# Kernel tuning notes

Hardware: AMD Instinct MI355X
Metric: run time of the kernel (lower is better)

The kernel has to match this reference:

```python
import jax, jax.numpy as jnp
import numpy as np

# ----- module constants (from init_kwargs) -----
N = 1024          # Np = [N, N]
NZ = 16           # number of slices (O.shape[3])
NA = 0.65         # objective NA
WL = 0.5          # wavelength (um)
PS = 6.5          # camera pixel size (um)
MAG = 20.0        # magnification
PS_EFF = PS / MAG
DZ = 10.0 * PS / MAG                 # slice spacing (code overwrites wl/na**2)
KAPPA = 2.0 * np.pi * DZ / WL        # imag part of self.k
K = np.complex64(1j * KAPPA)         # self.k as a complex scalar


def _grids():
    c = (np.arange(N) - N // 2) * PS_EFF
    xx, yy = np.meshgrid(c, c)                       # spatial grids
    f = (np.arange(N) - N // 2) / (PS_EFF * N)
    uxx, uyy = np.meshgrid(f, f)                     # frequency grids
    return xx, yy, uxx, uyy

_XX, _YY, _UXX, _UYY = _grids()
_URR = _UXX ** 2 + _UYY ** 2
_PC = (_URR < (NA / WL) ** 2).astype(np.float64)     # centered pupil


def _fresnel(dz):
    # genFrensel: band-limited angular-spectrum kernel, stored in fft order
    kz = np.sqrt(np.maximum(_PC * ((1.0 / WL) ** 2 - _URR), 0.0))
    kern = _PC * np.exp(1j * 2.0 * np.pi * dz * kz)
    return jnp.asarray(np.fft.fftshift(kern).astype(np.complex64))

PUPIL = jnp.asarray(np.fft.fftshift(_PC).astype(np.complex64))   # fft order
PROPKERN = _fresnel(DZ)
PROPKERN_FOCUS = _fresnel(-DZ * (NZ - 1) / 2.0)
XX = jnp.asarray(_XX, jnp.float32)
YY = jnp.asarray(_YY, jnp.float32)


def _prop(u, kern):
    # torch.fft / torch.ifft pair == unnormalized fft2 / normalized ifft2
    return jnp.fft.ifft2(jnp.fft.fft2(u) * kern)


def _plane_wave(na_illum):
    dfx = 1.0 / (PS_EFF * N)
    tilt = jnp.round((na_illum / WL) / dfx) * dfx    # snap tilt to freq grid
    phase = 2.0 * np.pi * (tilt[0] * XX + tilt[1] * YY)
    return jnp.exp(1j * phase)                        # complex64


def _ms_grad(O, intensity, na_illum):
    """Faithful translation of Multislice.grad. O: [N,N,NZ] complex64."""
    T = jnp.exp(K * O)                                # per-slice transmittance
    u = _plane_wave(na_illum)
    # forward multislice propagation
    for zz in range(NZ):
        u = T[..., zz] * u
        if zz < NZ - 1:
            u = _prop(u, PROPKERN)
    # refocus to stack center, apply pupil
    u_ref = _prop(u, PROPKERN_FOCUS)
    u_pup = _prop(u_ref, PUPIL)
    # amplitude-replacement residual
    abs_field = jnp.abs(u_pup)
    comp = jnp.sqrt(intensity) * u_pup / abs_field
    residual = u_pup - comp
    # back-propagate residual
    u_bp = _prop(residual, jnp.conj(PUPIL))
    u_bp = _prop(u_bp, jnp.conj(PROPKERN_FOCUS))
    # reverse slice loop accumulating per-slice gradient
    grads = [None] * NZ
    for zz in range(NZ - 1, -1, -1):
        grads[zz] = u_bp * jnp.conj(u) * jnp.conj(T[..., zz]) * np.conj(K)
        if zz > 0:
            u_bp = _prop(u_bp * jnp.conj(T[..., zz]), jnp.conj(PROPKERN))
            u = _prop(u, jnp.conj(PROPKERN))
            u = u / T[..., zz - 1]
    return jnp.stack(grads, axis=-1)                  # [N,N,NZ] complex


def setup_inputs() -> dict:
    key = jax.random.key(0)
    k1, k2, k3 = jax.random.split(key, 3)
    # small-valued object so exp(i*KAPPA*O) stays bounded (KAPPA ~ 40.8)
    x = jax.random.normal(k1, (N, N, 2, NZ), jnp.float32) * 0.01
    meas = jax.random.uniform(k2, (N, N), jnp.float32) + 0.1
    na_illum = jax.random.uniform(k3, (2,), jnp.float32) * 0.2
    alpha = jnp.full((1,), 0.01, jnp.float32)
    return {"x": x, "meas": meas, "na_illum": na_illum, "alpha": alpha}


def reference(x, meas, na_illum, alpha):
    # forward: x + step(x) = x - alpha * grad(x, meas, na_illum)
    O = x[..., 0, :] + 1j * x[..., 1, :]              # [N,N,NZ] complex64
    g = _ms_grad(O, meas, na_illum)
    out = O - alpha[0] * g
    return jnp.stack((out.real, out.imag), axis=2)    # back to [N,N,2,NZ]
```

## Files before the change

kernel.cpp:

```cpp
#include <hip/hip_runtime.h>
#include <math.h>


#define NN (1024*1024)
#define KAPPA 40.840704496667314f
#define TWO_PI_F 6.2831853071795865f
#define DFX_D 0.0030048076923076925
#define RRCUT 187177
#define F(i) ((i) + ((i)>>4))

#define JT 0
#define JT_WP 1
#define JN 2
#define JRESID 3

__device__ __forceinline__ float2 cmulf(float2 a, float2 b){
    return make_float2(a.x*b.x - a.y*b.y, a.x*b.y + a.y*b.x);
}
__device__ __forceinline__ float2 cmulcj(float2 a, float2 b){
    return make_float2(a.x*b.x + a.y*b.y, a.y*b.x - a.x*b.y);
}
__device__ __forceinline__ float2 f2add(float2 a, float2 b){ return make_float2(a.x+b.x, a.y+b.y); }
__device__ __forceinline__ float2 f2sub(float2 a, float2 b){ return make_float2(a.x-b.x, a.y-b.y); }

__device__ __forceinline__ void fill_tw(float2* tw, int tid){
    #pragma unroll
    for (int k = tid; k < 512; k += 256){
        float s, c; sincosf(-(float)k * (TWO_PI_F/1024.0f), &s, &c);
        tw[k] = make_float2(c, s);
    }
}

__device__ __forceinline__ void dif_ph1(float2 r[8], const float2* tw, int lane){
    float2 a, d;
    #pragma unroll
    for (int k=0;k<4;++k){
        a=r[k]; d=f2sub(r[k],r[k+4]);
        r[k]=f2add(a,r[k+4]);
        r[k+4]=cmulf(d, tw[lane+128*k]);
    }
    float2 w20 = tw[lane<<1], w21 = tw[(lane+128)<<1];
    a=r[0]; d=f2sub(r[0],r[2]); r[0]=f2add(a,r[2]); r[2]=cmulf(d,w20);
    a=r[1]; d=f2sub(r[1],r[3]); r[1]=f2add(a,r[3]); r[3]=cmulf(d,w21);
    a=r[4]; d=f2sub(r[4],r[6]); r[4]=f2add(a,r[6]); r[6]=cmulf(d,w20);
    a=r[5]; d=f2sub(r[5],r[7]); r[5]=f2add(a,r[7]); r[7]=cmulf(d,w21);
    float2 w3 = tw[lane<<2];
    a=r[0]; d=f2sub(r[0],r[1]); r[0]=f2add(a,r[1]); r[1]=cmulf(d,w3);
    a=r[2]; d=f2sub(r[2],r[3]); r[2]=f2add(a,r[3]); r[3]=cmulf(d,w3);
    a=r[4]; d=f2sub(r[4],r[5]); r[4]=f2add(a,r[5]); r[5]=cmulf(d,w3);
    a=r[6]; d=f2sub(r[6],r[7]); r[6]=f2add(a,r[7]); r[7]=cmulf(d,w3);
}
__device__ __forceinline__ void dit_ph1(float2 r[8], const float2* tw, int lane){
    float2 a, b;
    float2 w3 = tw[lane<<2];
    a=r[0]; b=cmulcj(r[1],w3); r[0]=f2add(a,b); r[1]=f2sub(a,b);
    a=r[2]; b=cmulcj(r[3],w3); r[2]=f2add(a,b); r[3]=f2sub(a,b);
    a=r[4]; b=cmulcj(r[5],w3); r[4]=f2add(a,b); r[5]=f2sub(a,b);
    a=r[6]; b=cmulcj(r[7],w3); r[6]=f2add(a,b); r[7]=f2sub(a,b);
    float2 w20 = tw[lane<<1], w21 = tw[(lane+128)<<1];
    a=r[0]; b=cmulcj(r[2],w20); r[0]=f2add(a,b); r[2]=f2sub(a,b);
    a=r[1]; b=cmulcj(r[3],w21); r[1]=f2add(a,b); r[3]=f2sub(a,b);
    a=r[4]; b=cmulcj(r[6],w20); r[4]=f2add(a,b); r[6]=f2sub(a,b);
    a=r[5]; b=cmulcj(r[7],w21); r[5]=f2add(a,b); r[7]=f2sub(a,b);
    #pragma unroll
    for (int k=0;k<4;++k){
        a=r[k]; b=cmulcj(r[k+4], tw[lane+128*k]);
        r[k]=f2add(a,b); r[k+4]=f2sub(a,b);
    }
}
__device__ __forceinline__ void dif_ph2(float2 r[8], const float2* tw, int m0){
    float2 a, d;
    #pragma unroll
    for (int k=0;k<4;++k){
        a=r[k]; d=f2sub(r[k],r[k+4]);
        r[k]=f2add(a,r[k+4]);
        r[k+4]=cmulf(d, tw[(m0+16*k)<<3]);
    }
    float2 w40 = tw[m0<<4], w41 = tw[(m0+16)<<4];
    a=r[0]; d=f2sub(r[0],r[2]); r[0]=f2add(a,r[2]); r[2]=cmulf(d,w40);
    a=r[1]; d=f2sub(r[1],r[3]); r[1]=f2add(a,r[3]); r[3]=cmulf(d,w41);
    a=r[4]; d=f2sub(r[4],r[6]); r[4]=f2add(a,r[6]); r[6]=cmulf(d,w40);
    a=r[5]; d=f2sub(r[5],r[7]); r[5]=f2add(a,r[7]); r[7]=cmulf(d,w41);
    float2 w5 = tw[m0<<5];
    a=r[0]; d=f2sub(r[0],r[1]); r[0]=f2add(a,r[1]); r[1]=cmulf(d,w5);
    a=r[2]; d=f2sub(r[2],r[3]); r[2]=f2add(a,r[3]); r[3]=cmulf(d,w5);
    a=r[4]; d=f2sub(r[4],r[5]); r[4]=f2add(a,r[5]); r[5]=cmulf(d,w5);
    a=r[6]; d=f2sub(r[6],r[7]); r[6]=f2add(a,r[7]); r[7]=cmulf(d,w5);
}
__device__ __forceinline__ void dit_ph2(float2 r[8], const float2* tw, int m0){
    float2 a, b;
    float2 w5 = tw[m0<<5];
    a=r[0]; b=cmulcj(r[1],w5); r[0]=f2add(a,b); r[1]=f2sub(a,b);
    a=r[2]; b=cmulcj(r[3],w5); r[2]=f2add(a,b); r[3]=f2sub(a,b);
    a=r[4]; b=cmulcj(r[5],w5); r[4]=f2add(a,b); r[5]=f2sub(a,b);
    a=r[6]; b=cmulcj(r[7],w5); r[6]=f2add(a,b); r[7]=f2sub(a,b);
    float2 w40 = tw[m0<<4], w41 = tw[(m0+16)<<4];
    a=r[0]; b=cmulcj(r[2],w40); r[0]=f2add(a,b); r[2]=f2sub(a,b);
    a=r[1]; b=cmulcj(r[3],w41); r[1]=f2add(a,b); r[3]=f2sub(a,b);
    a=r[4]; b=cmulcj(r[6],w40); r[4]=f2add(a,b); r[6]=f2sub(a,b);
    a=r[5]; b=cmulcj(r[7],w41); r[5]=f2add(a,b); r[7]=f2sub(a,b);
    #pragma unroll
    for (int k=0;k<4;++k){
        a=r[k]; b=cmulcj(r[k+4], tw[(m0+16*k)<<3]);
        r[k]=f2add(a,b); r[k+4]=f2sub(a,b);
    }
}
__device__ __forceinline__ void dif_reg(float2 r[8]){
    const float C = 0.70710678118654752f;
    float2 a,d;
    a=r[0]; d=f2sub(r[0],r[4]); r[0]=f2add(a,r[4]); r[4]=d;
    a=r[1]; d=f2sub(r[1],r[5]); r[1]=f2add(a,r[5]); r[5]=make_float2(C*(d.x+d.y), C*(d.y-d.x));
    a=r[2]; d=f2sub(r[2],r[6]); r[2]=f2add(a,r[6]); r[6]=make_float2(d.y, -d.x);
    a=r[3]; d=f2sub(r[3],r[7]); r[3]=f2add(a,r[7]); r[7]=make_float2(C*(d.y-d.x), -C*(d.x+d.y));
    a=r[0]; r[0]=f2add(a,r[2]); r[2]=f2sub(a,r[2]);
    a=r[1]; d=f2sub(r[1],r[3]); r[1]=f2add(a,r[3]); r[3]=make_float2(d.y,-d.x);
    a=r[4]; r[4]=f2add(a,r[6]); r[6]=f2sub(a,r[6]);
    a=r[5]; d=f2sub(r[5],r[7]); r[5]=f2add(a,r[7]); r[7]=make_float2(d.y,-d.x);
    a=r[0]; r[0]=f2add(a,r[1]); r[1]=f2sub(a,r[1]);
    a=r[2]; r[2]=f2add(a,r[3]); r[3]=f2sub(a,r[3]);
    a=r[4]; r[4]=f2add(a,r[5]); r[5]=f2sub(a,r[5]);
    a=r[6]; r[6]=f2add(a,r[7]); r[7]=f2sub(a,r[7]);
}
__device__ __forceinline__ void dit_reg(float2 r[8]){
    const float C = 0.70710678118654752f;
    float2 a,b,t;
    a=r[0]; r[0]=f2add(a,r[1]); r[1]=f2sub(a,r[1]);
    a=r[2]; r[2]=f2add(a,r[3]); r[3]=f2sub(a,r[3]);
    a=r[4]; r[4]=f2add(a,r[5]); r[5]=f2sub(a,r[5]);
    a=r[6]; r[6]=f2add(a,r[7]); r[7]=f2sub(a,r[7]);
    a=r[0]; r[0]=f2add(a,r[2]); r[2]=f2sub(a,r[2]);
    a=r[1]; t=r[3]; b=make_float2(-t.y, t.x); r[1]=f2add(a,b); r[3]=f2sub(a,b);
    a=r[4]; r[4]=f2add(a,r[6]); r[6]=f2sub(a,r[6]);
    a=r[5]; t=r[7]; b=make_float2(-t.y, t.x); r[5]=f2add(a,b); r[7]=f2sub(a,b);
    a=r[0]; r[0]=f2add(a,r[4]); r[4]=f2sub(a,r[4]);
    a=r[1]; t=r[5]; b=make_float2(C*(t.x-t.y), C*(t.x+t.y)); r[1]=f2add(a,b); r[5]=f2sub(a,b);
    a=r[2]; t=r[6]; b=make_float2(-t.y, t.x); r[2]=f2add(a,b); r[6]=f2sub(a,b);
    a=r[3]; t=r[7]; b=make_float2(-C*(t.x+t.y), C*(t.x-t.y)); r[3]=f2add(a,b); r[7]=f2sub(a,b);
}

__device__ __forceinline__ void st128l(float2* L, int ro, int lane, const float2 r[8]){
    #pragma unroll
    for (int k=0;k<8;++k) L[F(ro + lane + 128*k)] = r[k];
}
__device__ __forceinline__ void ld128l(const float2* L, int ro, int lane, float2 r[8]){
    #pragma unroll
    for (int k=0;k<8;++k) r[k] = L[F(ro + lane + 128*k)];
}
__device__ __forceinline__ void st16l(float2* L, int ro, int lane, const float2 r[8]){
    int b = lane>>4, m0 = lane&15, q = ro + 128*b + m0;
    #pragma unroll
    for (int k=0;k<8;++k) L[F(q + 16*k)] = r[k];
}
__device__ __forceinline__ void ld16l(const float2* L, int ro, int lane, float2 r[8]){
    int b = lane>>4, m0 = lane&15, q = ro + 128*b + m0;
    #pragma unroll
    for (int k=0;k<8;++k) r[k] = L[F(q + 16*k)];
}
__device__ __forceinline__ void st8l(float2* L, int ro, int lane, const float2 r[8]){
    int q = ro + 8*lane;
    #pragma unroll
    for (int i=0;i<8;++i) L[F(q + i)] = r[i];
}
__device__ __forceinline__ void ldfold_dif(const float2* L, int ro, int lane,
                                           const float2* tw, float2 r[8]){
    int rr = lane>>1, sub = lane&1, q = ro + 16*rr;
    #pragma unroll
    for (int i=0;i<8;++i){
        float2 x = L[F(q + i)];
        float2 y = L[F(q + 8 + i)];
        r[i] = sub ? cmulf(f2sub(x,y), tw[i<<6]) : f2add(x,y);
    }
}
__device__ __forceinline__ void ldfold_dit(const float2* L, int ro, int lane,
                                           const float2* tw, float2 r[8]){
    int b = lane>>4, m0 = lane&15, m0s = m0&7;
    float2 w = tw[m0s<<6];
    int q = ro + 128*b + m0s;
    #pragma unroll
    for (int k=0;k<8;++k){
        float2 x = L[F(q + 16*k)];
        float2 y = L[F(q + 16*k + 8)];
        float2 bb = cmulcj(y, w);
        r[k] = (m0 < 8) ? f2add(x,bb) : f2sub(x,bb);
    }
}
__device__ __forceinline__ void load8g(const float2* src, int lane, float2 r[8]){
    const float4* s4 = (const float4*)src + lane*4;
    #pragma unroll
    for (int m=0;m<4;++m){
        float4 v = s4[m];
        r[2*m]   = make_float2(v.x, v.y);
        r[2*m+1] = make_float2(v.z, v.w);
    }
}
__device__ __forceinline__ void twrite2(const float2* L, int tid, float2* dst,
                                        int r0, float s){
    #pragma unroll
    for (int k=0;k<4;++k){
        int c = tid + (k<<8);
        float2 a0 = L[F(c)], a1 = L[F(1024+c)];
        ((float4*)(dst + ((size_t)c<<10) + r0))[0] =
            make_float4(a0.x*s, a0.y*s, a1.x*s, a1.y*s);
    }
}

__global__ void __launch_bounds__(256) k_kern(float2* __restrict__ kp,
                                              float2* __restrict__ kf){
    int idx = blockIdx.x*256 + threadIdx.x;
    int j = idx >> 10, i = idx & 1023;
    int a = __brev((unsigned)i) >> 22;
    int b = __brev((unsigned)j) >> 22;
    int ra = a - (a >= 512 ? 1024 : 0);
    int rb = b - (b >= 512 ? 1024 : 0);
    int rr = ra*ra + rb*rb;
    float2 p = make_float2(0.f,0.f), f = make_float2(0.f,0.f);
    if (rr <= RRCUT){
        double urr = (double)rr * (DFX_D*DFX_D);
        double kz = sqrt(4.0 - urr);
        double s1,c1,s2,c2;
        sincos(6.283185307179586 * 3.25    * kz, &s1, &c1);
        sincos(6.283185307179586 * -24.375 * kz, &s2, &c2);
        p = make_float2((float)c1,(float)s1);
        f = make_float2((float)c2,(float)s2);
    }
    kp[idx] = p; kf[idx] = f;
}

__global__ void __launch_bounds__(256) k_T(const float4* __restrict__ x,
                                           float2* __restrict__ T){
    int idx = blockIdx.x*256 + threadIdx.x;
    const float4* xp = x + (size_t)idx*8;
    float4 v[8];
    #pragma unroll
    for (int k=0;k<8;++k) v[k] = xp[k];
    const float* fr = (const float*)v;
    #pragma unroll
    for (int z=0; z<16; ++z){
        float amp = __expf(-KAPPA*fr[16+z]);
        float s, c; __sincosf(KAPPA*fr[z], &s, &c);
        T[(size_t)z*NN + idx] = make_float2(amp*c, amp*s);
    }
}

__global__ void __launch_bounds__(256) k_head(float2* __restrict__ dst,
                                              const float2* __restrict__ T0,
                                              const float* __restrict__ nail){
    __shared__ float2 A[2176], B[2176], tw[512];
    const int tid = threadIdx.x;
    fill_tw(tw, tid);
    const int row = tid>>7, lane = tid&127, ro = row<<10, m0 = lane&15;
    const int r0 = blockIdx.x*2;
    const size_t gbase = ((size_t)(r0+row))<<10;
    float dfx = (float)DFX_D;
    float t0 = rintf(nail[0]*2.0f/dfx)*dfx;
    float t1 = rintf(nail[1]*2.0f/dfx)*dfx;
    float yv = (float)((r0+row) - 512) * 0.325f;
    float2 r[8];
    #pragma unroll
    for (int k=0;k<8;++k){
        int col = lane + 128*k;
        float2 tv = T0[gbase + col];
        float xv = (float)(col - 512) * 0.325f;
        float s0, c0; sincosf(TWO_PI_F*(t0*xv + t1*yv), &s0, &c0);
        r[k] = cmulf(make_float2(c0,s0), tv);
    }
    __syncthreads();
    dif_ph1(r, tw, lane);
    st128l(A, ro, lane, r); __syncthreads();
    ld16l(A, ro, lane, r); dif_ph2(r, tw, m0);
    st16l(B, ro, lane, r); __syncthreads();
    ldfold_dif(B, ro, lane, tw, r); dif_reg(r);
    st8l(A, ro, lane, r); __syncthreads();
    twrite2(A, tid, dst, r0, 1.0f);
}

__global__ void __launch_bounds__(256) k_pass2(
    const float2* __restrict__ srcA, float2* __restrict__ dstA,
    const float2* __restrict__ srcB, float2* __restrict__ dstB,
    const float2* __restrict__ km, int conj, int pupil)
{
    __shared__ float2 A[2176], B[2176], tw[512];
    const int tid = threadIdx.x;
    fill_tw(tw, tid);
    const int row = tid>>7, lane = tid&127, ro = row<<10, m0 = lane&15;
    int bid = blockIdx.x;
    const float2* src = srcA; float2* dst = dstA;
    if (srcB != nullptr && bid >= 512){ src = srcB; dst = dstB; bid -= 512; }
    const int r0 = bid*2;
    const int jrow = r0 + row;
    const float2* srcR = src + (((size_t)r0)<<10) + ro;
    float2 r[8];
    #pragma unroll
    for (int k=0;k<8;++k) r[k] = srcR[lane + 128*k];
    __syncthreads();
    dif_ph1(r, tw, lane);
    st128l(A, ro, lane, r); __syncthreads();
    ld16l(A, ro, lane, r); dif_ph2(r, tw, m0);
    st16l(B, ro, lane, r); __syncthreads();
    ldfold_dif(B, ro, lane, tw, r); dif_reg(r);
    if (pupil){
        int bb = __brev((unsigned)jrow) >> 22;
        int rb = bb - (bb >= 512 ? 1024 : 0);
        int rb2 = rb*rb;
        #pragma unroll
        for (int i=0;i<8;++i){
            int aa = __brev((unsigned)(8*lane+i)) >> 22;
            int ra = aa - (aa >= 512 ? 1024 : 0);
            if (ra*ra + rb2 > RRCUT) r[i] = make_float2(0.f,0.f);
        }
    } else {
        const float4* k4 = (const float4*)(km + (((size_t)jrow)<<10)) + lane*4;
        float sg = conj ? -1.0f : 1.0f;
        #pragma unroll
        for (int m=0;m<4;++m){
            float4 kv = k4[m];
            r[2*m]   = cmulf(r[2*m],   make_float2(kv.x, sg*kv.y));
            r[2*m+1] = cmulf(r[2*m+1], make_float2(kv.z, sg*kv.w));
        }
    }
    dit_reg(r);
    st8l(A, ro, lane, r); __syncthreads();
    ldfold_dit(A, ro, lane, tw, r); dit_ph2(r, tw, m0);
    st16l(B, ro, lane, r); __syncthreads();
    ld128l(B, ro, lane, r); dit_ph1(r, tw, lane);
    st128l(A, ro, lane, r); __syncthreads();
    twrite2(A, tid, dst, r0, 1.0f/1024.0f);
}

__global__ void __launch_bounds__(256) k_junc(
    const float2* __restrict__ src, float2* __restrict__ dst,
    const float2* __restrict__ Tz, float2* __restrict__ wp,
    const float* __restrict__ meas, int mode)
{
    __shared__ float2 A[2176], B[2176], tw[512];
    const int tid = threadIdx.x;
    fill_tw(tw, tid);
    const int row = tid>>7, lane = tid&127, ro = row<<10, m0 = lane&15;
    const int r0 = blockIdx.x*2;
    const size_t gbase = ((size_t)(r0+row))<<10;
    const float S = 1.0f/1024.0f;
    float2 r[8];
    load8g(src + (((size_t)r0)<<10) + ro, lane, r);
    dit_reg(r);
    st8l(A, ro, lane, r); __syncthreads();
    ldfold_dit(A, ro, lane, tw, r); dit_ph2(r, tw, m0);
    st16l(B, ro, lane, r); __syncthreads();
    ld128l(B, ro, lane, r); dit_ph1(r, tw, lane);
    #pragma unroll
    for (int k=0;k<8;++k){
        size_t g = gbase + lane + 128*k;
        float2 v = make_float2(S*r[k].x, S*r[k].y);
        if (mode == JT || mode == JT_WP){
            v = cmulf(v, Tz[g]);
            if (mode == JT_WP) wp[g] = v;
        } else if (mode == JRESID){
            float m = meas[g];
            float aamp = fmaxf(sqrtf(v.x*v.x + v.y*v.y), 1e-30f);
            float f = 1.0f - sqrtf(m)/aamp;
            v.x *= f; v.y *= f;
        }
        r[k] = v;
    }
    dif_ph1(r, tw, lane);
    st128l(A, ro, lane, r); __syncthreads();
    ld16l(A, ro, lane, r); dif_ph2(r, tw, m0);
    st16l(B, ro, lane, r); __syncthreads();
    ldfold_dif(B, ro, lane, tw, r); dif_reg(r);
    st8l(A, ro, lane, r); __syncthreads();
    twrite2(A, tid, dst, r0, 1.0f);
}

__global__ void __launch_bounds__(256) k_rev(
    const float2* __restrict__ srcU, float2* __restrict__ dstU,
    const float2* __restrict__ srcB, float2* __restrict__ dstB,
    float2* __restrict__ Tz, int headU)
{
    __shared__ float2 A[2176], B[2176], tw[512];
    const int tid = threadIdx.x;
    fill_tw(tw, tid);
    const int row = tid>>7, lane = tid&127, ro = row<<10, m0 = lane&15;
    const int r0 = blockIdx.x*2;
    const size_t gbase = ((size_t)(r0+row))<<10;
    const float S = 1.0f/1024.0f;
    float2 u[8], Tg[8], r[8];
    if (!headU){
        load8g(srcU + (((size_t)r0)<<10) + ro, lane, u);
        dit_reg(u);
        st8l(A, ro, lane, u); __syncthreads();
        ldfold_dit(A, ro, lane, tw, u); dit_ph2(u, tw, m0);
        st16l(B, ro, lane, u); __syncthreads();
        ld128l(B, ro, lane, u); dit_ph1(u, tw, lane);
        #pragma unroll
        for (int k=0;k<8;++k){ u[k].x *= S; u[k].y *= S; }
    } else {
        const float2* srcR = srcU + (((size_t)r0)<<10) + ro;
        #pragma unroll
        for (int k=0;k<8;++k) u[k] = srcR[lane + 128*k];
        __syncthreads();
    }
    #pragma unroll
    for (int k=0;k<8;++k) Tg[k] = Tz[gbase + lane + 128*k];
    #pragma unroll
    for (int k=0;k<8;++k){
        if (headU) r[k] = u[k];
        else {
            float inv = 1.0f/(Tg[k].x*Tg[k].x + Tg[k].y*Tg[k].y);
            float2 wc = cmulcj(u[k], Tg[k]);
            r[k] = make_float2(wc.x*inv, wc.y*inv);
        }
    }
    dif_ph1(r, tw, lane);
    st128l(A, ro, lane, r); __syncthreads();
    ld16l(A, ro, lane, r); dif_ph2(r, tw, m0);
    st16l(B, ro, lane, r); __syncthreads();
    ldfold_dif(B, ro, lane, tw, r); dif_reg(r);
    st8l(A, ro, lane, r); __syncthreads();
    twrite2(A, tid, dstU, r0, 1.0f);
    load8g(srcB + (((size_t)r0)<<10) + ro, lane, r);
    dit_reg(r);
    st8l(B, ro, lane, r); __syncthreads();
    ldfold_dit(B, ro, lane, tw, r); dit_ph2(r, tw, m0);
    st16l(A, ro, lane, r); __syncthreads();
    ld128l(A, ro, lane, r); dit_ph1(r, tw, lane);
    #pragma unroll
    for (int k=0;k<8;++k){
        float2 b = make_float2(S*r[k].x, S*r[k].y);
        float2 q = headU ? cmulcj(cmulcj(b, u[k]), Tg[k]) : cmulcj(b, u[k]);
        Tz[gbase + lane + 128*k] = make_float2(KAPPA*q.y, -KAPPA*q.x);
        r[k] = cmulcj(b, Tg[k]);
    }
    dif_ph1(r, tw, lane);
    st128l(B, ro, lane, r); __syncthreads();
    ld16l(B, ro, lane, r); dif_ph2(r, tw, m0);
    st16l(A, ro, lane, r); __syncthreads();
    ldfold_dif(A, ro, lane, tw, r); dif_reg(r);
    st8l(B, ro, lane, r); __syncthreads();
    twrite2(B, tid, dstB, r0, 1.0f);
}

__global__ void __launch_bounds__(256) k_tail(
    const float2* __restrict__ srcU, const float2* __restrict__ srcB,
    float2* __restrict__ G0)
{
    __shared__ float2 A[2176], B[2176], tw[512];
    const int tid = threadIdx.x;
    fill_tw(tw, tid);
    const int row = tid>>7, lane = tid&127, ro = row<<10, m0 = lane&15;
    const int r0 = blockIdx.x*2;
    const size_t gbase = ((size_t)(r0+row))<<10;
    const float S = 1.0f/1024.0f;
    float2 u[8], r[8];
    load8g(srcU + (((size_t)r0)<<10) + ro, lane, u);
    dit_reg(u);
    st8l(A, ro, lane, u); __syncthreads();
    ldfold_dit(A, ro, lane, tw, u); dit_ph2(u, tw, m0);
    st16l(B, ro, lane, u); __syncthreads();
    ld128l(B, ro, lane, u); dit_ph1(u, tw, lane);
    load8g(srcB + (((size_t)r0)<<10) + ro, lane, r);
    dit_reg(r);
    st8l(A, ro, lane, r); __syncthreads();
    ldfold_dit(A, ro, lane, tw, r); dit_ph2(r, tw, m0);
    st16l(B, ro, lane, r); __syncthreads();
    ld128l(B, ro, lane, r); dit_ph1(r, tw, lane);
    #pragma unroll
    for (int k=0;k<8;++k){
        float2 b = make_float2(S*r[k].x, S*r[k].y);
        float2 w = make_float2(S*u[k].x, S*u[k].y);
        float2 q = cmulcj(b, w);
        G0[gbase + lane + 128*k] = make_float2(KAPPA*q.y, -KAPPA*q.x);
    }
}

__global__ void __launch_bounds__(256) k_merge(const float4* __restrict__ x,
                                               const float2* __restrict__ G,
                                               const float* __restrict__ alpha,
                                               float4* __restrict__ out){
    int idx = blockIdx.x*256 + threadIdx.x;
    float al = alpha[0];
    const float4* xp = x + (size_t)idx*8;
    float4 xv[8];
    #pragma unroll
    for (int k=0;k<8;++k) xv[k] = xp[k];
    const float* fx = (const float*)xv;
    float o[32];
    #pragma unroll
    for (int z=0;z<16;++z){
        float2 g = G[(size_t)z*NN + idx];
        o[z]    = fx[z]    - al*g.x;
        o[16+z] = fx[16+z] - al*g.y;
    }
    float4* op = out + (size_t)idx*8;
    #pragma unroll
    for (int k=0;k<8;++k)
        op[k] = make_float4(o[4*k], o[4*k+1], o[4*k+2], o[4*k+3]);
}

extern "C" void kernel_launch(void* const* d_in, const int* in_sizes, int n_in,
                              void* d_out, int out_size, void* d_ws, size_t ws_size,
                              hipStream_t stream)
{
    const float* x     = (const float*)d_in[0];
    const float* meas  = (const float*)d_in[1];
    const float* nail  = (const float*)d_in[2];
    const float* alpha = (const float*)d_in[3];

    if (ws_size < (size_t)23*NN*sizeof(float2)) return;

    float2* W   = (float2*)d_ws;
    float2* T   = W;
    float2* KP  = W + (size_t)16*NN;
    float2* KF  = W + (size_t)17*NN;
    float2* U0  = W + (size_t)18*NN;
    float2* TAB = W + (size_t)19*NN;
    float2* TBB = W + (size_t)20*NN;
    float2* TAU = W + (size_t)21*NN;
    float2* TBU = W + (size_t)22*NN;

    k_kern<<<4096, 256, 0, stream>>>(KP, KF);
    k_T   <<<4096, 256, 0, stream>>>((const float4*)x, T);

    auto P2f = [&](const float2* km, int cj, int pup){
        k_pass2<<<512, 256, 0, stream>>>(TAB, TBB, nullptr, nullptr, km, cj, pup);
    };

    k_head<<<512, 256, 0, stream>>>(TAB, T, nail);
    P2f(KP, 0, 0);
    for (int z = 1; z <= 14; ++z){
        k_junc<<<512, 256, 0, stream>>>(TBB, TAB, T + (size_t)z*NN, nullptr, nullptr, JT);
        P2f(KP, 0, 0);
    }
    k_junc<<<512, 256, 0, stream>>>(TBB, TAB, T + (size_t)15*NN, U0, nullptr, JT_WP);
    P2f(KF, 0, 0);
    k_junc<<<512, 256, 0, stream>>>(TBB, TAB, nullptr, nullptr, nullptr, JN);
    P2f(nullptr, 0, 1);
    k_junc<<<512, 256, 0, stream>>>(TBB, TAB, nullptr, nullptr, meas, JRESID);
    P2f(nullptr, 1, 1);
    k_junc<<<512, 256, 0, stream>>>(TBB, TAB, nullptr, nullptr, nullptr, JN);
    P2f(KF, 1, 0);

    for (int zz = 15; zz >= 1; --zz){
        k_rev<<<512, 256, 0, stream>>>(zz == 15 ? U0 : TBU, TAU, TBB, TAB,
                                       T + (size_t)zz*NN, zz == 15 ? 1 : 0);
        k_pass2<<<1024, 256, 0, stream>>>(TAB, TBB, TAU, TBU, KP, 1, 0);
    }
    k_tail<<<512, 256, 0, stream>>>(TBU, TBB, T);

    k_merge<<<4096, 256, 0, stream>>>((const float4*)x, T, alpha, (float4*)d_out);
}
```

Measured before the change: 1.514 ms.

## Hoist global loads ahead of LDS FFT stages and widen elementwise kernels

Global loads of kernel coefficients, transmittance, measurements and the second FFT operand are issued before the shared-memory FFT phases in pass2, junc, rev and tail. Their latency can then overlap with compute and barriers instead of stalling afterwards. The T and merge kernels are rewritten so each thread handles a quarter or eighth of a pixel's slices, giving more threads and better-coalesced loads. The cost is higher register pressure from the extra live arrays, which may reduce occupancy.

```diff
diff --git a/kernel.cpp b/kernel.cpp
--- a/kernel.cpp
+++ b/kernel.cpp
@@ -229,16 +229,18 @@
 __global__ void __launch_bounds__(256) k_T(const float4* __restrict__ x,
                                            float2* __restrict__ T){
     int idx = blockIdx.x*256 + threadIdx.x;
-    const float4* xp = x + (size_t)idx*8;
-    float4 v[8];
-    #pragma unroll
-    for (int k=0;k<8;++k) v[k] = xp[k];
-    const float* fr = (const float*)v;
-    #pragma unroll
-    for (int z=0; z<16; ++z){
-        float amp = __expf(-KAPPA*fr[16+z]);
-        float s, c; __sincosf(KAPPA*fr[z], &s, &c);
-        T[(size_t)z*NN + idx] = make_float2(amp*c, amp*s);
+    int p = idx >> 2;
+    int q = idx & 3;
+    float4 vr = x[(size_t)p*8 + q];
+    float4 vi = x[(size_t)p*8 + 4 + q];
+    const float* fr = (const float*)&vr;
+    const float* fi = (const float*)&vi;
+    #pragma unroll
+    for (int j=0;j<4;++j){
+        int z = 4*q + j;
+        float amp = __expf(-KAPPA*fi[j]);
+        float s, c; __sincosf(KAPPA*fr[j], &s, &c);
+        T[(size_t)z*NN + p] = make_float2(amp*c, amp*s);
     }
 }
 
@@ -292,6 +294,12 @@
     float2 r[8];
     #pragma unroll
     for (int k=0;k<8;++k) r[k] = srcR[lane + 128*k];
+    float4 kv[4];
+    if (!pupil){
+        const float4* k4 = (const float4*)(km + (((size_t)jrow)<<10)) + lane*4;
+        #pragma unroll
+        for (int m=0;m<4;++m) kv[m] = k4[m];
+    }
     __syncthreads();
     dif_ph1(r, tw, lane);
     st128l(A, ro, lane, r); __syncthreads();
@@ -309,13 +317,11 @@
             if (ra*ra + rb2 > RRCUT) r[i] = make_float2(0.f,0.f);
         }
     } else {
-        const float4* k4 = (const float4*)(km + (((size_t)jrow)<<10)) + lane*4;
         float sg = conj ? -1.0f : 1.0f;
         #pragma unroll
         for (int m=0;m<4;++m){
-            float4 kv = k4[m];
-            r[2*m]   = cmulf(r[2*m],   make_float2(kv.x, sg*kv.y));
-            r[2*m+1] = cmulf(r[2*m+1], make_float2(kv.z, sg*kv.w));
+            r[2*m]   = cmulf(r[2*m],   make_float2(kv[m].x, sg*kv[m].y));
+            r[2*m+1] = cmulf(r[2*m+1], make_float2(kv[m].z, sg*kv[m].w));
         }
     }
     dit_reg(r);
@@ -341,6 +347,14 @@
     const float S = 1.0f/1024.0f;
     float2 r[8];
     load8g(src + (((size_t)r0)<<10) + ro, lane, r);
+    float2 pre[8];
+    if (mode == JT || mode == JT_WP){
+        #pragma unroll
+        for (int k=0;k<8;++k) pre[k] = Tz[gbase + lane + 128*k];
+    } else if (mode == JRESID){
+        #pragma unroll
+        for (int k=0;k<8;++k) pre[k].x = meas[gbase + lane + 128*k];
+    }
     dit_reg(r);
     st8l(A, ro, lane, r); __syncthreads();
     ldfold_dit(A, ro, lane, tw, r); dit_ph2(r, tw, m0);
@@ -351,10 +365,10 @@
         size_t g = gbase + lane + 128*k;
         float2 v = make_float2(S*r[k].x, S*r[k].y);
         if (mode == JT || mode == JT_WP){
-            v = cmulf(v, Tz[g]);
+            v = cmulf(v, pre[k]);
             if (mode == JT_WP) wp[g] = v;
         } else if (mode == JRESID){
-            float m = meas[g];
+            float m = pre[k].x;
             float aamp = fmaxf(sqrtf(v.x*v.x + v.y*v.y), 1e-30f);
             float f = 1.0f - sqrtf(m)/aamp;
             v.x *= f; v.y *= f;
@@ -382,9 +396,18 @@
     const int r0 = blockIdx.x*2;
     const size_t gbase = ((size_t)(r0+row))<<10;
     const float S = 1.0f/1024.0f;
-    float2 u[8], Tg[8], r[8];
+    float2 u[8], Tg[8], bb[8], r[8];
     if (!headU){
         load8g(srcU + (((size_t)r0)<<10) + ro, lane, u);
+    } else {
+        const float2* srcR = srcU + (((size_t)r0)<<10) + ro;
+        #pragma unroll
+        for (int k=0;k<8;++k) u[k] = srcR[lane + 128*k];
+    }
+    #pragma unroll
+    for (int k=0;k<8;++k) Tg[k] = Tz[gbase + lane + 128*k];
+    load8g(srcB + (((size_t)r0)<<10) + ro, lane, bb);
+    if (!headU){
         dit_reg(u);
         st8l(A, ro, lane, u); __syncthreads();
         ldfold_dit(A, ro, lane, tw, u); dit_ph2(u, tw, m0);
@@ -393,13 +416,8 @@
         #pragma unroll
         for (int k=0;k<8;++k){ u[k].x *= S; u[k].y *= S; }
     } else {
-        const float2* srcR = srcU + (((size_t)r0)<<10) + ro;
-        #pragma unroll
-        for (int k=0;k<8;++k) u[k] = srcR[lane + 128*k];
         __syncthreads();
     }
-    #pragma unroll
-    for (int k=0;k<8;++k) Tg[k] = Tz[gbase + lane + 128*k];
     #pragma unroll
     for (int k=0;k<8;++k){
         if (headU) r[k] = u[k];
@@ -416,9 +434,8 @@
     ldfold_dif(B, ro, lane, tw, r); dif_reg(r);
     st8l(A, ro, lane, r); __syncthreads();
     twrite2(A, tid, dstU, r0, 1.0f);
-    load8g(srcB + (((size_t)r0)<<10) + ro, lane, r);
-    dit_reg(r);
-    st8l(B, ro, lane, r); __syncthreads();
+    dit_reg(bb);
+    st8l(B, ro, lane, bb); __syncthreads();
     ldfold_dit(B, ro, lane, tw, r); dit_ph2(r, tw, m0);
     st16l(A, ro, lane, r); __syncthreads();
     ld128l(A, ro, lane, r); dit_ph1(r, tw, lane);
@@ -451,12 +468,12 @@
     const float S = 1.0f/1024.0f;
     float2 u[8], r[8];
     load8g(srcU + (((size_t)r0)<<10) + ro, lane, u);
+    load8g(srcB + (((size_t)r0)<<10) + ro, lane, r);
     dit_reg(u);
     st8l(A, ro, lane, u); __syncthreads();
     ldfold_dit(A, ro, lane, tw, u); dit_ph2(u, tw, m0);
     st16l(B, ro, lane, u); __syncthreads();
     ld128l(B, ro, lane, u); dit_ph1(u, tw, lane);
-    load8g(srcB + (((size_t)r0)<<10) + ro, lane, r);
     dit_reg(r);
     st8l(A, ro, lane, r); __syncthreads();
     ldfold_dit(A, ro, lane, tw, r); dit_ph2(r, tw, m0);
@@ -475,24 +492,21 @@
                                                const float2* __restrict__ G,
                                                const float* __restrict__ alpha,
                                                float4* __restrict__ out){
-    int idx = blockIdx.x*256 + threadIdx.x;
+    int idx4 = blockIdx.x*256 + threadIdx.x;
+    int p  = idx4 >> 3;
+    int f  = idx4 & 7;
+    int c  = f >> 2;
+    int zb = (f & 3) * 4;
     float al = alpha[0];
-    const float4* xp = x + (size_t)idx*8;
-    float4 xv[8];
-    #pragma unroll
-    for (int k=0;k<8;++k) xv[k] = xp[k];
-    const float* fx = (const float*)xv;
-    float o[32];
-    #pragma unroll
-    for (int z=0;z<16;++z){
-        float2 g = G[(size_t)z*NN + idx];
-        o[z]    = fx[z]    - al*g.x;
-        o[16+z] = fx[16+z] - al*g.y;
-    }
-    float4* op = out + (size_t)idx*8;
-    #pragma unroll
-    for (int k=0;k<8;++k)
-        op[k] = make_float4(o[4*k], o[4*k+1], o[4*k+2], o[4*k+3]);
+    float4 xv = x[idx4];
+    float gc[4];
+    #pragma unroll
+    for (int j=0;j<4;++j){
+        float2 g = G[(size_t)(zb + j)*NN + p];
+        gc[j] = c ? g.y : g.x;
+    }
+    out[idx4] = make_float4(xv.x - al*gc[0], xv.y - al*gc[1],
+                            xv.z - al*gc[2], xv.w - al*gc[3]);
 }
 
 extern "C" void kernel_launch(void* const* d_in, const int* in_sizes, int n_in,
@@ -517,7 +531,7 @@
     float2* TBU = W + (size_t)22*NN;
 
     k_kern<<<4096, 256, 0, stream>>>(KP, KF);
-    k_T   <<<4096, 256, 0, stream>>>((const float4*)x, T);
+    k_T   <<<16384, 256, 0, stream>>>((const float4*)x, T);
 
     auto P2f = [&](const float2* km, int cj, int pup){
         k_pass2<<<512, 256, 0, stream>>>(TAB, TBB, nullptr, nullptr, km, cj, pup);
@@ -545,5 +559,5 @@
     }
     k_tail<<<512, 256, 0, stream>>>(TBU, TBB, T);
 
-    k_merge<<<4096, 256, 0, stream>>>((const float4*)x, T, alpha, (float4*)d_out);
-}
+    k_merge<<<32768, 256, 0, stream>>>((const float4*)x, T, alpha, (float4*)d_out);
+}
```

Result: faster. 1.461 ms (-3.6%).
